# Kernel tuning notes

Hardware: AMD Instinct MI355X
Metric: run time of the kernel (lower is better)

The kernel has to match this reference:

```python
import jax, jax.numpy as jnp
import numpy as np

B, S, D, MAX_LEN = 8, 2048, 512, 2048
NEG_INF = jnp.float32(-jnp.inf)


def setup_inputs() -> dict:
    key = jax.random.key(0)
    ks = jax.random.split(key, 10)
    s = 1.0 / np.sqrt(D)
    inp = {
        "x": jax.random.normal(ks[0], (B, S, D), dtype=jnp.float32),
        "pos_table": jax.random.normal(ks[1], (MAX_LEN, D), dtype=jnp.float32) * 0.02,
        "Wq": jax.random.normal(ks[2], (D, D), dtype=jnp.float32) * s,
        "bq": jnp.zeros((D,), dtype=jnp.float32),
        "Wk": jax.random.normal(ks[3], (D, D), dtype=jnp.float32) * s,
        "bk": jnp.zeros((D,), dtype=jnp.float32),
        "Wv": jax.random.normal(ks[4], (D, D), dtype=jnp.float32) * s,
        "bv": jnp.zeros((D,), dtype=jnp.float32),
        "Wd": jax.random.normal(ks[5], (D, D), dtype=jnp.float32) * s,
        "bd": jnp.zeros((D,), dtype=jnp.float32),
    }
    return inp


def reference(x, pos_table, Wq, bq, Wk, bk, Wv, bv, Wd, bd):
    # add learned positional embeddings (add_pos=True path): arange over seq dim
    x = x + pos_table[:x.shape[-2]]  # [B,S,D]
    # torch nn.Linear: y = x @ W.T + b
    q = jnp.einsum("bsd,ed->bse", x, Wq) + bq
    k = jnp.einsum("bsd,ed->bse", x, Wk) + bk
    v = jnp.einsum("bsd,ed->bse", x, Wv) + bv
    v = jnp.where(jnp.isnan(v), 0.0, v)  # nan_to_num(nan=0)
    scale = 1.0 / jnp.sqrt(jnp.float32(D))
    scores = jnp.einsum("bqd,bkd->bqk", q, k) * scale  # [B,S,S]
    scores = jnp.where(jnp.isnan(scores), NEG_INF, scores)  # nan_to_num(nan=-inf)
    attn = jax.nn.softmax(scores, axis=2)
    y = jnp.einsum("bqk,bkd->bqd", attn, v)
    return jnp.einsum("bsd,ed->bse", y, Wd) + bd
```

## Files before the change

kernel.cpp:

```cpp
#include <hip/hip_runtime.h>
#include <stdint.h>

typedef __bf16 bf16x8 __attribute__((ext_vector_type(8)));
typedef float f32x4 __attribute__((ext_vector_type(4)));

static constexpr float QK_SCALE = 0.044194173824159216f;

__device__ __forceinline__ uint16_t f2bf(float f) {
    uint32_t x = __builtin_bit_cast(uint32_t, f);
    x += 0x7FFFu + ((x >> 16) & 1u);
    return (uint16_t)(x >> 16);
}

__device__ __forceinline__ void cp16(const uint16_t* g, uint16_t* l) {
    __builtin_amdgcn_global_load_lds(
        (__attribute__((address_space(1))) void*)(uint16_t*)g,
        (__attribute__((address_space(3))) void*)l,
        16, 0, 0);
}

template <int MODE>
__global__ __launch_bounds__(256, 3) void gemm_nt(
    const uint16_t* __restrict__ A, const uint16_t* __restrict__ Bm,
    void* __restrict__ C0, void* __restrict__ C1, void* __restrict__ C2,
    const float* __restrict__ bias0, const float* __restrict__ bias1,
    const float* __restrict__ bias2,
    float scale, int K, int ldc, long bsA, long bsB, long bsC,
    int scols, int stPerBatch)
{
    __shared__ __align__(16) uint16_t SH[3][8192];

    const uint32_t id  = blockIdx.x;
    const uint32_t xcd = id & 7u;
    const uint32_t p   = id >> 3;
    const uint32_t q   = p >> 4;
    const uint32_t w   = p & 15u;
    const uint32_t g   = q * 8u + xcd;
    const uint32_t bz  = g / (uint32_t)stPerBatch;
    const uint32_t gs  = g - bz * (uint32_t)stPerBatch;
    const uint32_t sr  = gs / (uint32_t)scols;
    const uint32_t sc  = gs - sr * (uint32_t)scols;
    const int bm = (int)(sr * 4u + (w >> 2));
    const int bn = (int)(sc * 4u + (w & 3u));

    const int t  = threadIdx.x;
    const int wave = t >> 6, lane = t & 63;
    const int wm = (wave >> 1) * 64, wn = (wave & 1) * 64;
    const int lm = lane & 15, lq = lane >> 4;
    const int sw = lq ^ ((lm >> 1) & 3);

    const uint16_t* Ab = A  + (long)bz * bsA + (long)bm * 128 * K;
    const uint16_t* Bb = Bm + (long)bz * bsB + (long)bn * 128 * K;

    long goff[2]; int loff[2];
#pragma unroll
    for (int j = 0; j < 2; ++j) {
        const int s  = j * 256 + t;
        const int r  = s >> 2;
        const int cs = s & 3;
        const int cg = cs ^ ((r >> 1) & 3);
        goff[j] = (long)r * K + cg * 8;
        loff[j] = s * 8;
    }

    const int KI = K >> 5;

#pragma unroll
    for (int st = 0; st < 2; ++st)
#pragma unroll
        for (int j = 0; j < 2; ++j) {
            cp16(Ab + goff[j] + st * 32, SH[st] + loff[j]);
            cp16(Bb + goff[j] + st * 32, SH[st] + 4096 + loff[j]);
        }

    f32x4 acc[4][4] = {};
    float rsum[4] = {0.f, 0.f, 0.f, 0.f};

    int cur = 0, pf = 2;
    for (int k = 0; k < KI; ++k) {
        asm volatile("s_waitcnt vmcnt(4) lgkmcnt(0)\n\ts_barrier" ::: "memory");

        int kp = k + 2; if (kp >= KI) kp = KI - 1;
        uint16_t* dst = SH[pf];
        const long ko = (long)kp * 32;
#pragma unroll
        for (int j = 0; j < 2; ++j) {
            cp16(Ab + goff[j] + ko, dst + loff[j]);
            cp16(Bb + goff[j] + ko, dst + 4096 + loff[j]);
        }

        const uint16_t* buf = SH[cur];
        bf16x8 af[4], bfr[4];
#pragma unroll
        for (int i = 0; i < 4; ++i)
            af[i]  = *(const bf16x8*)&buf[((wm + i * 16 + lm) * 4 + sw) * 8];
#pragma unroll
        for (int i = 0; i < 4; ++i)
            bfr[i] = *(const bf16x8*)&buf[4096 + ((wn + i * 16 + lm) * 4 + sw) * 8];

        if (MODE == 5) {
#pragma unroll
            for (int j = 0; j < 4; ++j) {
                const uint4 u = __builtin_bit_cast(uint4, af[j]);
                float s0 = __builtin_bit_cast(float, u.x << 16)
                         + __builtin_bit_cast(float, u.x & 0xFFFF0000u);
                float s1 = __builtin_bit_cast(float, u.y << 16)
                         + __builtin_bit_cast(float, u.y & 0xFFFF0000u);
                float s2 = __builtin_bit_cast(float, u.z << 16)
                         + __builtin_bit_cast(float, u.z & 0xFFFF0000u);
                float s3 = __builtin_bit_cast(float, u.w << 16)
                         + __builtin_bit_cast(float, u.w & 0xFFFF0000u);
                rsum[j] += (s0 + s1) + (s2 + s3);
            }
        }

#pragma unroll
        for (int i = 0; i < 4; ++i)
#pragma unroll
            for (int j = 0; j < 4; ++j)
                acc[i][j] = __builtin_amdgcn_mfma_f32_16x16x32_bf16(
                    bfr[i], af[j], acc[i][j], 0, 0, 0);

        cur = (cur == 2) ? 0 : cur + 1;
        pf  = (pf  == 2) ? 0 : pf  + 1;
    }

    float inv[4];
    if (MODE == 5) {
#pragma unroll
        for (int j = 0; j < 4; ++j) {
            float s = rsum[j];
            s += __shfl_xor(s, 16);
            s += __shfl_xor(s, 32);
            inv[j] = 1.f / s;
        }
    }

    const int mb = bm * 128 + wm + lm;
    const int nb = bn * 128 + wn + lq * 4;
#pragma unroll
    for (int i = 0; i < 4; ++i) {
        const int n = nb + i * 16;
        if (MODE == 0 || MODE == 4 || MODE == 5) {
#pragma unroll
            for (int j = 0; j < 4; ++j) {
                const int m = mb + j * 16;
                float v0, v1, v2, v3;
                if (MODE == 4) {
                    v0 = __expf(acc[i][j][0] * scale);
                    v1 = __expf(acc[i][j][1] * scale);
                    v2 = __expf(acc[i][j][2] * scale);
                    v3 = __expf(acc[i][j][3] * scale);
                } else if (MODE == 5) {
                    v0 = acc[i][j][0] * inv[j];
                    v1 = acc[i][j][1] * inv[j];
                    v2 = acc[i][j][2] * inv[j];
                    v3 = acc[i][j][3] * inv[j];
                } else {
                    v0 = acc[i][j][0] * scale;
                    v1 = acc[i][j][1] * scale;
                    v2 = acc[i][j][2] * scale;
                    v3 = acc[i][j][3] * scale;
                }
                const uint32_t lo = (uint32_t)f2bf(v0) | ((uint32_t)f2bf(v1) << 16);
                const uint32_t hi = (uint32_t)f2bf(v2) | ((uint32_t)f2bf(v3) << 16);
                *(uint2*)&((uint16_t*)C0)[(long)bz * bsC + (long)m * ldc + n] =
                    make_uint2(lo, hi);
            }
        } else if (MODE == 2) {
            const float4 b4 = *(const float4*)&bias0[n];
#pragma unroll
            for (int j = 0; j < 4; ++j) {
                const int m = mb + j * 16;
                *(float4*)&((float*)C0)[(long)m * ldc + n] = make_float4(
                    acc[i][j][0] + b4.x, acc[i][j][1] + b4.y,
                    acc[i][j][2] + b4.z, acc[i][j][3] + b4.w);
            }
        } else {
            const int sec = n >> 9, nn = n & 511;
            const float* bp = sec == 0 ? bias0 : (sec == 1 ? bias1 : bias2);
            const float4 b4 = *(const float4*)&bp[nn];
#pragma unroll
            for (int j = 0; j < 4; ++j) {
                const int m = mb + j * 16;
                if (sec < 2) {
                    uint16_t* Cq = (uint16_t*)(sec == 0 ? C0 : C1);
                    const uint32_t lo = (uint32_t)f2bf(acc[i][j][0] + b4.x) |
                                        ((uint32_t)f2bf(acc[i][j][1] + b4.y) << 16);
                    const uint32_t hi = (uint32_t)f2bf(acc[i][j][2] + b4.z) |
                                        ((uint32_t)f2bf(acc[i][j][3] + b4.w) << 16);
                    *(uint2*)&Cq[(long)m * 512 + nn] = make_uint2(lo, hi);
                } else {
                    const int bb = m >> 11, ss = m & 2047;
                    uint16_t* vt = (uint16_t*)C2 + ((long)bb * 512 + nn) * 2048 + ss;
                    vt[0]        = f2bf(acc[i][j][0] + b4.x);
                    vt[2048]     = f2bf(acc[i][j][1] + b4.y);
                    vt[2 * 2048] = f2bf(acc[i][j][2] + b4.z);
                    vt[3 * 2048] = f2bf(acc[i][j][3] + b4.w);
                }
            }
        }
    }
}

__global__ __launch_bounds__(256) void prep_x(const float* __restrict__ x,
                                              const float* __restrict__ pos,
                                              uint16_t* __restrict__ xb)
{
    const long i8 = ((long)blockIdx.x * 256 + threadIdx.x) * 8;
    const long p8 = i8 & ((1l << 20) - 1);
    const float4* xv = (const float4*)(x + i8);
    const float4* pv = (const float4*)(pos + p8);
    const float4 a0 = xv[0], a1 = xv[1];
    const float4 b0 = pv[0], b1 = pv[1];
    uint16_t o[8];
    o[0] = f2bf(a0.x + b0.x); o[1] = f2bf(a0.y + b0.y);
    o[2] = f2bf(a0.z + b0.z); o[3] = f2bf(a0.w + b0.w);
    o[4] = f2bf(a1.x + b1.x); o[5] = f2bf(a1.y + b1.y);
    o[6] = f2bf(a1.z + b1.z); o[7] = f2bf(a1.w + b1.w);
    *(uint4*)(xb + i8) = *(uint4*)o;
}

__global__ __launch_bounds__(256) void prep_w(
    const float* __restrict__ Wq, const float* __restrict__ Wk,
    const float* __restrict__ Wv, const float* __restrict__ Wd,
    uint16_t* __restrict__ wqkv, uint16_t* __restrict__ wd)
{
    const long f = ((long)blockIdx.x * 256 + threadIdx.x) * 8;
    const int  w = (int)(f >> 18);
    const long off = f & 262143;
    const float* src = (w == 0) ? Wq : (w == 1) ? Wk : (w == 2) ? Wv : Wd;
    uint16_t* dst = (w < 3) ? (wqkv + (long)w * 262144 + off) : (wd + off);
    const float4* s4 = (const float4*)(src + off);
    const float4 a = s4[0], b = s4[1];
    uint16_t o[8];
    o[0] = f2bf(a.x); o[1] = f2bf(a.y); o[2] = f2bf(a.z); o[3] = f2bf(a.w);
    o[4] = f2bf(b.x); o[5] = f2bf(b.y); o[6] = f2bf(b.z); o[7] = f2bf(b.w);
    *(uint4*)dst = *(uint4*)o;
}

extern "C" void kernel_launch(void* const* d_in, const int* in_sizes, int n_in,
                              void* d_out, int out_size, void* d_ws, size_t ws_size,
                              hipStream_t stream)
{
    const float* x   = (const float*)d_in[0];
    const float* pos = (const float*)d_in[1];
    const float* Wq  = (const float*)d_in[2];
    const float* bq  = (const float*)d_in[3];
    const float* Wk  = (const float*)d_in[4];
    const float* bk  = (const float*)d_in[5];
    const float* Wv  = (const float*)d_in[6];
    const float* bv  = (const float*)d_in[7];
    const float* Wd  = (const float*)d_in[8];
    const float* bd  = (const float*)d_in[9];
    float* out = (float*)d_out;

    char* ws = (char*)d_ws;
    uint16_t* xb   = (uint16_t*)(ws);
    uint16_t* wqkv = (uint16_t*)(ws + 16777216);
    uint16_t* wd   = (uint16_t*)(ws + 18350080);
    uint16_t* Qb   = (uint16_t*)(ws + 18874368);
    uint16_t* Kb   = (uint16_t*)(ws + 35651584);
    uint16_t* Vt   = (uint16_t*)(ws + 52428800);
    uint16_t* Pb   = (uint16_t*)(ws + 69206016);
    uint16_t* yb   = (uint16_t*)(ws + 136314880);

    prep_x<<<4096, 256, 0, stream>>>(x, pos, xb);
    prep_w<<<512, 256, 0, stream>>>(Wq, Wk, Wv, Wd, wqkv, wd);

    gemm_nt<3><<<1536, 256, 0, stream>>>(
        xb, wqkv, Qb, Kb, Vt, bq, bk, bv, 1.0f, 512, 512, 0, 0, 0, 3, 96);

    gemm_nt<4><<<2048, 256, 0, stream>>>(
        Qb, Kb, Pb, nullptr, nullptr, nullptr, nullptr, nullptr,
        QK_SCALE, 512, 2048, (long)2048 * 512, (long)2048 * 512,
        (long)2048 * 2048, 4, 16);

    gemm_nt<5><<<512, 256, 0, stream>>>(
        Pb, Vt, yb, nullptr, nullptr, nullptr, nullptr, nullptr,
        1.0f, 2048, 512, (long)2048 * 2048, (long)512 * 2048,
        (long)2048 * 512, 1, 4);

    gemm_nt<2><<<512, 256, 0, stream>>>(
        yb, wd, out, nullptr, nullptr, bd, nullptr, nullptr,
        1.0f, 512, 512, 0, 0, 0, 1, 32);
}
```

Baseline: 270.8 us.

## Add 256x256-tile 8-wave GEMM kernel for the QK^T exp-scores stage

Introduces a new 512-thread GEMM kernel with 256x256 output tiles, a triple-buffered LDS pipeline, and barrier-interleaved prefetch. The QK^T + exp stage now uses it instead of the 128x128 kernel. The larger tiles are meant to raise data reuse per global load and cut the block count. The cost is higher register pressure (128 accumulators per thread) and lower occupancy, along with a new block-to-XCD mapping.

```diff
diff --git a/kernel.cpp b/kernel.cpp
--- a/kernel.cpp
+++ b/kernel.cpp
@@ -141,17 +141,12 @@
 #pragma unroll
     for (int i = 0; i < 4; ++i) {
         const int n = nb + i * 16;
-        if (MODE == 0 || MODE == 4 || MODE == 5) {
+        if (MODE == 0 || MODE == 5) {
 #pragma unroll
             for (int j = 0; j < 4; ++j) {
                 const int m = mb + j * 16;
                 float v0, v1, v2, v3;
-                if (MODE == 4) {
-                    v0 = __expf(acc[i][j][0] * scale);
-                    v1 = __expf(acc[i][j][1] * scale);
-                    v2 = __expf(acc[i][j][2] * scale);
-                    v3 = __expf(acc[i][j][3] * scale);
-                } else if (MODE == 5) {
+                if (MODE == 5) {
                     v0 = acc[i][j][0] * inv[j];
                     v1 = acc[i][j][1] * inv[j];
                     v2 = acc[i][j][2] * inv[j];
@@ -203,6 +198,134 @@
     }
 }
 
+template <int MODE>
+__global__ __launch_bounds__(512, 2) void gemm_nt8(
+    const uint16_t* __restrict__ A, const uint16_t* __restrict__ Bm,
+    void* __restrict__ C0,
+    float scale, int K, int ldc, long bsA, long bsB, long bsC,
+    int scols, int stPerBatch)
+{
+    __shared__ __align__(16) uint16_t SH[3][16384];
+
+    const uint32_t id  = blockIdx.x;
+    const uint32_t xcd = id & 7u;
+    const uint32_t p   = id >> 3;
+    const uint32_t q   = p >> 4;
+    const uint32_t w   = p & 15u;
+    const uint32_t g   = q * 8u + xcd;
+    const uint32_t bz  = g / (uint32_t)stPerBatch;
+    const uint32_t gs  = g - bz * (uint32_t)stPerBatch;
+    const uint32_t sr  = gs / (uint32_t)scols;
+    const uint32_t sc  = gs - sr * (uint32_t)scols;
+    const int bm = (int)(sr * 4u + (w >> 2));
+    const int bn = (int)(sc * 4u + (w & 3u));
+
+    const int t  = threadIdx.x;
+    const int wave = t >> 6, lane = t & 63;
+    const int wm2 = (wave >> 2) * 128;
+    const int wn2 = (wave & 3) * 64;
+    const int lm = lane & 15, lq = lane >> 4;
+    const int sw = lq ^ ((lm >> 1) & 3);
+
+    const uint16_t* Ab = A  + (long)bz * bsA + (long)bm * 256 * K;
+    const uint16_t* Bb = Bm + (long)bz * bsB + (long)bn * 256 * K;
+
+    long goff[2]; int loff[2];
+#pragma unroll
+    for (int j = 0; j < 2; ++j) {
+        const int s  = j * 512 + t;
+        const int r  = s >> 2;
+        const int cs = s & 3;
+        const int cg = cs ^ ((r >> 1) & 3);
+        goff[j] = (long)r * K + cg * 8;
+        loff[j] = s * 8;
+    }
+
+    const int KI = K >> 5;
+
+#pragma unroll
+    for (int st = 0; st < 2; ++st)
+#pragma unroll
+        for (int j = 0; j < 2; ++j) {
+            cp16(Ab + goff[j] + st * 32, SH[st] + loff[j]);
+            cp16(Bb + goff[j] + st * 32, SH[st] + 8192 + loff[j]);
+        }
+    asm volatile("s_waitcnt vmcnt(4)\n\ts_barrier" ::: "memory");
+
+    f32x4 acc[4][8] = {};
+
+    int cur = 0, pf = 2;
+    for (int k = 0; k < KI; ++k) {
+        int kp = k + 2; if (kp >= KI) kp = KI - 1;
+        uint16_t* dst = SH[pf];
+        const long ko = (long)kp * 32;
+        const uint16_t* buf = SH[cur];
+
+        bf16x8 af[8], bfr[4];
+#define RDA(jj) (*(const bf16x8*)&buf[((wm2 + (jj) * 16 + lm) * 4 + sw) * 8])
+#define RDB(ii) (*(const bf16x8*)&buf[8192 + ((wn2 + (ii) * 16 + lm) * 4 + sw) * 8])
+#define MFMA8(pp)                                                              \
+    __builtin_amdgcn_s_setprio(1);                                             \
+    _Pragma("unroll")                                                          \
+    for (int i = 0; i < 4; ++i) {                                              \
+        acc[i][2 * (pp)]     = __builtin_amdgcn_mfma_f32_16x16x32_bf16(        \
+            bfr[i], af[2 * (pp)],     acc[i][2 * (pp)],     0, 0, 0);          \
+        acc[i][2 * (pp) + 1] = __builtin_amdgcn_mfma_f32_16x16x32_bf16(        \
+            bfr[i], af[2 * (pp) + 1], acc[i][2 * (pp) + 1], 0, 0, 0);          \
+    }                                                                          \
+    __builtin_amdgcn_s_setprio(0);
+
+        bfr[0] = RDB(0); bfr[1] = RDB(1); bfr[2] = RDB(2); bfr[3] = RDB(3);
+        af[0] = RDA(0); af[1] = RDA(1);
+        cp16(Ab + goff[0] + ko, dst + loff[0]);
+        MFMA8(0);
+        asm volatile("s_barrier" ::: "memory");
+        af[2] = RDA(2); af[3] = RDA(3);
+        cp16(Ab + goff[1] + ko, dst + loff[1]);
+        MFMA8(1);
+        asm volatile("s_barrier" ::: "memory");
+        af[4] = RDA(4); af[5] = RDA(5);
+        cp16(Bb + goff[0] + ko, dst + 8192 + loff[0]);
+        MFMA8(2);
+        asm volatile("s_barrier" ::: "memory");
+        af[6] = RDA(6); af[7] = RDA(7);
+        cp16(Bb + goff[1] + ko, dst + 8192 + loff[1]);
+        MFMA8(3);
+        asm volatile("s_waitcnt vmcnt(4) lgkmcnt(0)\n\ts_barrier" ::: "memory");
+#undef RDA
+#undef RDB
+#undef MFMA8
+
+        cur = (cur == 2) ? 0 : cur + 1;
+        pf  = (pf  == 2) ? 0 : pf  + 1;
+    }
+
+    const int mb = bm * 256 + wm2 + lm;
+    const int nb = bn * 256 + wn2 + lq * 4;
+#pragma unroll
+    for (int i = 0; i < 4; ++i) {
+        const int n = nb + i * 16;
+#pragma unroll
+        for (int j = 0; j < 8; ++j) {
+            const int m = mb + j * 16;
+            float v0, v1, v2, v3;
+            if (MODE == 4) {
+                v0 = __expf(acc[i][j][0] * scale);
+                v1 = __expf(acc[i][j][1] * scale);
+                v2 = __expf(acc[i][j][2] * scale);
+                v3 = __expf(acc[i][j][3] * scale);
+            } else {
+                v0 = acc[i][j][0] * scale; v1 = acc[i][j][1] * scale;
+                v2 = acc[i][j][2] * scale; v3 = acc[i][j][3] * scale;
+            }
+            const uint32_t lo = (uint32_t)f2bf(v0) | ((uint32_t)f2bf(v1) << 16);
+            const uint32_t hi = (uint32_t)f2bf(v2) | ((uint32_t)f2bf(v3) << 16);
+            *(uint2*)&((uint16_t*)C0)[(long)bz * bsC + (long)m * ldc + n] =
+                make_uint2(lo, hi);
+        }
+    }
+}
+
 __global__ __launch_bounds__(256) void prep_x(const float* __restrict__ x,
                                               const float* __restrict__ pos,
                                               uint16_t* __restrict__ xb)
@@ -271,10 +394,9 @@
     gemm_nt<3><<<1536, 256, 0, stream>>>(
         xb, wqkv, Qb, Kb, Vt, bq, bk, bv, 1.0f, 512, 512, 0, 0, 0, 3, 96);
 
-    gemm_nt<4><<<2048, 256, 0, stream>>>(
-        Qb, Kb, Pb, nullptr, nullptr, nullptr, nullptr, nullptr,
-        QK_SCALE, 512, 2048, (long)2048 * 512, (long)2048 * 512,
-        (long)2048 * 2048, 4, 16);
+    gemm_nt8<4><<<512, 512, 0, stream>>>(
+        Qb, Kb, Pb, QK_SCALE, 512, 2048, (long)2048 * 512, (long)2048 * 512,
+        (long)2048 * 2048, 2, 4);
 
     gemm_nt<5><<<512, 256, 0, stream>>>(
         Pb, Vt, yb, nullptr, nullptr, nullptr, nullptr, nullptr,
```

New measurement: 265.1 us. -2.1%, faster.
